# Optimization experiments

Measured on AMD Instinct MI355X. Metric: run time of the kernel, lower is better.

The kernel has to match this reference:

```python
import jax, jax.numpy as jnp
from jax import lax
import numpy as np

B = 2; Hs = 48; Ws = 48
DIM = 768; NH = 6; NP = 4; DH = DIM // NH; HID = int(DIM * 0.25)
LIN = Hs * Ws                    # feat tokens (single deform level)
LQ = 21 * (Hs * Ws) // 4         # query tokens: (2H*2W)+(H*W)+(H/2*W/2)


def _ln(x, g, b, eps=1e-6):
    m = jnp.mean(x, -1, keepdims=True)
    v = jnp.mean((x - m) ** 2, -1, keepdims=True)
    return (x - m) * lax.rsqrt(v + eps) * g + b


def _bilinear_sample(value, loc, Hf, Wf):
    """value: [B,NH,Hf*Wf,DH]; loc: [B,Lq,NH,NP,2] normalized to [0,1].
    Matches F.grid_sample(align_corners=False, padding_mode='zeros')."""
    Bq, nH = value.shape[0], value.shape[1]
    Lq = loc.shape[1]
    x = loc[..., 0] * Wf - 0.5
    y = loc[..., 1] * Hf - 0.5
    x0 = jnp.floor(x); y0 = jnp.floor(y)
    wx1 = x - x0; wy1 = y - y0
    x0i = x0.astype(jnp.int32); y0i = y0.astype(jnp.int32)

    def tr(a):  # [B,Lq,NH,NP] -> [B,NH,Lq*NP]
        return jnp.transpose(a, (0, 2, 1, 3)).reshape(Bq, nH, Lq * NP)

    def gather(yi, xi):
        valid = ((xi >= 0) & (xi < Wf) & (yi >= 0) & (yi < Hf)).astype(value.dtype)
        idx = jnp.clip(yi, 0, Hf - 1) * Wf + jnp.clip(xi, 0, Wf - 1)
        g = jnp.take_along_axis(value, tr(idx)[..., None], axis=2)  # [B,NH,Lq*NP,DH]
        return g * tr(valid)[..., None]

    out = (gather(y0i, x0i) * tr((1 - wy1) * (1 - wx1))[..., None]
         + gather(y0i, x0i + 1) * tr((1 - wy1) * wx1)[..., None]
         + gather(y0i + 1, x0i) * tr(wy1 * (1 - wx1))[..., None]
         + gather(y0i + 1, x0i + 1) * tr(wy1 * wx1)[..., None])
    return out.reshape(Bq, nH, Lq, NP, DH)


def _dwconv(x_tokens, w, b, h, w_):
    Bq, n_tok, C = x_tokens.shape
    img = jnp.transpose(x_tokens, (0, 2, 1)).reshape(Bq, C, h, w_)
    y = lax.conv_general_dilated(img, w, (1, 1), 'SAME',
                                 dimension_numbers=('NCHW', 'OIHW', 'NCHW'),
                                 feature_group_count=C) + b[None, :, None, None]
    return jnp.transpose(y.reshape(Bq, C, h * w_), (0, 2, 1))


def _forward(query, reference_points, feat, qn_g, qn_b, fn_g, fn_b, vW, vb,
             soW, sob, awW, awb, opW, opb, mn_g, mn_b,
             fc1W, fc1b, dwW, dwb, fc2W, fc2b, H, W):
    Bq, Lq, C = query.shape
    q = _ln(query, qn_g, qn_b)
    v = _ln(feat, fn_g, fn_b) @ vW + vb                             # [B,Lin,C]
    value = jnp.transpose(v.reshape(Bq, -1, NH, DH), (0, 2, 1, 3))  # [B,NH,Lin,DH]
    offs = (q @ soW + sob).reshape(Bq, Lq, NH, NP, 2)
    attw = jax.nn.softmax((q @ awW + awb).reshape(Bq, Lq, NH, NP), axis=-1)
    norm = jnp.asarray([W, H], dtype=q.dtype)                       # (x,y) normalizer
    loc = reference_points.reshape(Bq, Lq, 1, 1, 2) + offs / norm   # [B,Lq,NH,NP,2]
    samp = _bilinear_sample(value, loc, H, W)                       # [B,NH,Lq,NP,DH]
    aw = jnp.transpose(attw, (0, 2, 1, 3))[..., None]               # [B,NH,Lq,NP,1]
    out = jnp.sum(samp * aw, axis=3)                                # [B,NH,Lq,DH]
    out = jnp.transpose(out, (0, 2, 1, 3)).reshape(Bq, Lq, C) @ opW + opb
    x = query + out                                                 # residual
    # multi-scale conv MLP
    h = _ln(x, mn_g, mn_b) @ fc1W + fc1b                            # [B,Lq,HID]
    n = Lq // 21
    h = jnp.concatenate([
        _dwconv(h[:, :16 * n], dwW, dwb, 2 * H, 2 * W),
        _dwconv(h[:, 16 * n:20 * n], dwW, dwb, H, W),
        _dwconv(h[:, 20 * n:], dwW, dwb, H // 2, W // 2)], axis=1)
    h = jax.nn.gelu(h, approximate=False)
    h = h @ fc2W + fc2b
    return x + h


def setup_inputs():
    key = jax.random.key(0)
    ks = jax.random.split(key, 16)
    s = 0.02
    return dict(
        query=jax.random.normal(ks[0], (B, LQ, DIM), jnp.float32),
        reference_points=jax.random.uniform(ks[1], (B, LQ, 1, 2), jnp.float32),
        feat=jax.random.normal(ks[2], (B, LIN, DIM), jnp.float32),
        spatial_shapes=jnp.array([[Hs, Ws]], jnp.int32),
        level_start_index=jnp.array([0], jnp.int32),
        H=Hs, W=Ws,
        qn_g=jnp.ones((DIM,)), qn_b=jnp.zeros((DIM,)),
        fn_g=jnp.ones((DIM,)), fn_b=jnp.zeros((DIM,)),
        mn_g=jnp.ones((DIM,)), mn_b=jnp.zeros((DIM,)),
        vW=s * jax.random.normal(ks[3], (DIM, DIM)), vb=jnp.zeros((DIM,)),
        soW=s * jax.random.normal(ks[4], (DIM, NH * NP * 2)),
        sob=0.5 * jax.random.normal(ks[5], (NH * NP * 2,)),
        awW=s * jax.random.normal(ks[6], (DIM, NH * NP)), awb=jnp.zeros((NH * NP,)),
        opW=s * jax.random.normal(ks[7], (DIM, DIM)), opb=jnp.zeros((DIM,)),
        fc1W=s * jax.random.normal(ks[8], (DIM, HID)), fc1b=jnp.zeros((HID,)),
        dwW=s * jax.random.normal(ks[9], (HID, 1, 3, 3)), dwb=jnp.zeros((HID,)),
        fc2W=s * jax.random.normal(ks[10], (HID, DIM)), fc2b=jnp.zeros((DIM,)),
    )


def reference(query, reference_points, feat, spatial_shapes, level_start_index, H, W,
              qn_g, qn_b, fn_g, fn_b, mn_g, mn_b, vW, vb, soW, sob, awW, awb,
              opW, opb, fc1W, fc1b, dwW, dwb, fc2W, fc2b):
    del spatial_shapes, level_start_index  # single level; H,W are static ints
    return _forward(query, reference_points, feat, qn_g, qn_b, fn_g, fn_b, vW, vb,
                    soW, sob, awW, awb, opW, opb, mn_g, mn_b,
                    fc1W, fc1b, dwW, dwb, fc2W, fc2b, H, W)
```

## Files before the change

kernel.cpp:

```cpp
#include <hip/hip_runtime.h>

#define NB    2
#define LQT   12096
#define LINT  2304
#define DIMC  768
#define NHD   6
#define NPT   4
#define DHD   128
#define HIDC  192
#define HH    48
#define WW    48

typedef __attribute__((ext_vector_type(8))) short bf16x8;
typedef __attribute__((ext_vector_type(4))) float f32x4;
typedef __attribute__((ext_vector_type(8))) unsigned short u16x8;

__device__ __forceinline__ unsigned short f2bf(float f) {
  unsigned int u = __builtin_bit_cast(unsigned int, f);
  u += 0x7FFFu + ((u >> 16) & 1u);
  return (unsigned short)(u >> 16);
}

__global__ __launch_bounds__(256) void pack_wt(const float* __restrict__ src,
                                               unsigned short* __restrict__ dst,
                                               int K, int N, int rows) {
  size_t i = (size_t)blockIdx.x * 256 + threadIdx.x;
  if (i >= (size_t)rows * K) return;
  int n = (int)(i / K), k = (int)(i % K);
  float v = (n < N) ? src[(size_t)k * N + n] : 0.f;
  dst[i] = f2bf(v);
}

__global__ __launch_bounds__(256) void pack_soaw(const float* __restrict__ soW,
                                                 const float* __restrict__ awW,
                                                 const float* __restrict__ sob,
                                                 const float* __restrict__ awb,
                                                 unsigned short* __restrict__ dst,
                                                 float* __restrict__ bdst) {
  size_t i = (size_t)blockIdx.x * 256 + threadIdx.x;
  if (i < 128) bdst[i] = (i < 48) ? sob[i] : (i < 72 ? awb[i - 48] : 0.f);
  if (i >= (size_t)128 * DIMC) return;
  int n = (int)(i / DIMC), k = (int)(i % DIMC);
  float v = (n < 48) ? soW[(size_t)k * 48 + n]
                     : (n < 72 ? awW[(size_t)k * 24 + (n - 48)] : 0.f);
  dst[i] = f2bf(v);
}

__global__ __launch_bounds__(256) void ln_to_bf16(const float* __restrict__ in,
                                                  const float* __restrict__ gamma,
                                                  const float* __restrict__ beta,
                                                  unsigned short* __restrict__ out) {
  const int row = blockIdx.x;
  const int t = threadIdx.x;
  const float* x = in + (size_t)row * DIMC;
  float v0 = x[t], v1 = x[t + 256], v2 = x[t + 512];
  float s = v0 + v1 + v2;
  float s2 = v0 * v0 + v1 * v1 + v2 * v2;
#pragma unroll
  for (int o = 32; o > 0; o >>= 1) {
    s += __shfl_down(s, o);
    s2 += __shfl_down(s2, o);
  }
  __shared__ float red[8];
  const int wave = t >> 6, lane = t & 63;
  if (lane == 0) { red[wave] = s; red[wave + 4] = s2; }
  __syncthreads();
  float S = red[0] + red[1] + red[2] + red[3];
  float S2 = red[4] + red[5] + red[6] + red[7];
  float mean = S * (1.0f / DIMC);
  float var = S2 * (1.0f / DIMC) - mean * mean;
  float inv = rsqrtf(var + 1e-6f);
  unsigned short* o0 = out + (size_t)row * DIMC;
  o0[t]       = f2bf((v0 - mean) * inv * gamma[t]       + beta[t]);
  o0[t + 256] = f2bf((v1 - mean) * inv * gamma[t + 256] + beta[t + 256]);
  o0[t + 512] = f2bf((v2 - mean) * inv * gamma[t + 512] + beta[t + 512]);
}

#define LDSS 40
template <bool HAS_ADD>
__global__ __launch_bounds__(256) void gemm_bt(const unsigned short* __restrict__ A,
                                               const unsigned short* __restrict__ Bt,
                                               const float* __restrict__ bias,
                                               const float* __restrict__ add,
                                               float* __restrict__ out,
                                               int M, int N, int K) {
  __shared__ unsigned short As[128 * LDSS];
  __shared__ unsigned short Bs[128 * LDSS];
  const int t = threadIdx.x;
  const int wave = t >> 6, lane = t & 63;
  const int m0 = blockIdx.x * 128;
  const int n0 = blockIdx.y * 128;
  const int wm = (wave >> 1) * 64, wn = (wave & 1) * 64;
  const int lr = lane & 15;
  const int lk = (lane >> 4) * 8;

  const int e0 = t * 8;
  const int r0 = e0 >> 5;
  const int c0 = e0 & 31;

  const size_t arow0 = (size_t)(m0 + r0) * K;
  const size_t arow1 = (size_t)(m0 + r0 + 64) * K;
  const size_t brow0 = (size_t)(n0 + r0) * K;
  const size_t brow1 = (size_t)(n0 + r0 + 64) * K;

  f32x4 acc[4][4] = {};

  for (int k0 = 0; k0 < K; k0 += 32) {
    u16x8 a0 = *(const u16x8*)(A + arow0 + k0 + c0);
    u16x8 a1 = *(const u16x8*)(A + arow1 + k0 + c0);
    u16x8 b0 = *(const u16x8*)(Bt + brow0 + k0 + c0);
    u16x8 b1 = *(const u16x8*)(Bt + brow1 + k0 + c0);
    __syncthreads();
    *(u16x8*)(As + (size_t)r0 * LDSS + c0) = a0;
    *(u16x8*)(As + (size_t)(r0 + 64) * LDSS + c0) = a1;
    *(u16x8*)(Bs + (size_t)r0 * LDSS + c0) = b0;
    *(u16x8*)(Bs + (size_t)(r0 + 64) * LDSS + c0) = b1;
    __syncthreads();
    bf16x8 af[4], bg[4];
#pragma unroll
    for (int i = 0; i < 4; ++i)
      af[i] = *(const bf16x8*)(As + (size_t)(wm + i * 16 + lr) * LDSS + lk);
#pragma unroll
    for (int j = 0; j < 4; ++j)
      bg[j] = *(const bf16x8*)(Bs + (size_t)(wn + j * 16 + lr) * LDSS + lk);
#pragma unroll
    for (int i = 0; i < 4; ++i)
#pragma unroll
      for (int j = 0; j < 4; ++j)
        acc[i][j] = __builtin_amdgcn_mfma_f32_16x16x32_bf16(af[i], bg[j], acc[i][j], 0, 0, 0);
  }

  const int orow = (lane >> 4) * 4;
#pragma unroll
  for (int i = 0; i < 4; ++i) {
#pragma unroll
    for (int j = 0; j < 4; ++j) {
      const int n = n0 + wn + j * 16 + lr;
      if (n < N) {
#pragma unroll
        for (int r = 0; r < 4; ++r) {
          const int m = m0 + wm + i * 16 + orow + r;
          float v = acc[i][j][r] + bias[n];
          if (HAS_ADD) v += add[(size_t)m * N + n];
          out[(size_t)m * N + n] = v;
        }
      }
    }
  }
}

__global__ __launch_bounds__(192) void deform_attn(const float* __restrict__ soaw,
                                                   const float* __restrict__ rp,
                                                   const float* __restrict__ value,
                                                   unsigned short* __restrict__ attn) {
  const int row = blockIdx.x;
  const int b = row / LQT;
  const int t = threadIdx.x;
  const int h = t >> 5;
  const int l = t & 31;
  const float* sa = soaw + (size_t)row * 128;
  const float bx = rp[(size_t)row * 2 + 0] * (float)WW - 0.5f;
  const float by = rp[(size_t)row * 2 + 1] * (float)HH - 0.5f;

  float lg0 = sa[48 + h * 4 + 0], lg1 = sa[48 + h * 4 + 1];
  float lg2 = sa[48 + h * 4 + 2], lg3 = sa[48 + h * 4 + 3];
  float mx = fmaxf(fmaxf(lg0, lg1), fmaxf(lg2, lg3));
  float e0 = expf(lg0 - mx), e1 = expf(lg1 - mx), e2 = expf(lg2 - mx), e3 = expf(lg3 - mx);
  float inv = 1.0f / (e0 + e1 + e2 + e3);
  float awp[4] = {e0 * inv, e1 * inv, e2 * inv, e3 * inv};

  const float* vb = value + (size_t)b * LINT * DIMC + h * DHD + l * 4;
  float ax = 0.f, ay = 0.f, az = 0.f, aw = 0.f;
#pragma unroll
  for (int p = 0; p < 4; ++p) {
    float fx = bx + sa[h * 8 + p * 2 + 0];
    float fy = by + sa[h * 8 + p * 2 + 1];
    float x0f = floorf(fx), y0f = floorf(fy);
    float wx = fx - x0f, wy = fy - y0f;
    int x0 = (int)x0f, y0 = (int)y0f;
#pragma unroll
    for (int dy = 0; dy < 2; ++dy) {
#pragma unroll
      for (int dx = 0; dx < 2; ++dx) {
        int xi = x0 + dx, yi = y0 + dy;
        float w = (dy ? wy : 1.f - wy) * (dx ? wx : 1.f - wx) * awp[p];
        if (xi < 0 || xi >= WW || yi < 0 || yi >= HH) w = 0.f;
        int xc = min(max(xi, 0), WW - 1), yc = min(max(yi, 0), HH - 1);
        const float4 g = *(const float4*)(vb + (size_t)(yc * WW + xc) * DIMC);
        ax += w * g.x; ay += w * g.y; az += w * g.z; aw += w * g.w;
      }
    }
  }
  unsigned short* op = attn + (size_t)row * DIMC + h * DHD + l * 4;
  ushort4 ov;
  ov.x = f2bf(ax); ov.y = f2bf(ay); ov.z = f2bf(az); ov.w = f2bf(aw);
  *(ushort4*)op = ov;
}

__global__ __launch_bounds__(192) void dwconv_gelu(const float* __restrict__ h1,
                                                   const float* __restrict__ dwW,
                                                   const float* __restrict__ dwb,
                                                   unsigned short* __restrict__ out) {
  const int blk = blockIdx.x;
  const int b = blk / LQT;
  const int q = blk % LQT;
  int base, Wi, Hi;
  if (q < 9216)       { base = 0;     Wi = 96; Hi = 96; }
  else if (q < 11520) { base = 9216;  Wi = 48; Hi = 48; }
  else                { base = 11520; Wi = 24; Hi = 24; }
  const int loc = q - base;
  const int y = loc / Wi, x = loc % Wi;
  const int c = threadIdx.x;
  const float* src = h1 + ((size_t)b * LQT + base) * HIDC + c;
  float acc = dwb[c];
#pragma unroll
  for (int dy = -1; dy <= 1; ++dy) {
    int yy = y + dy;
    if (yy < 0 || yy >= Hi) continue;
#pragma unroll
    for (int dx = -1; dx <= 1; ++dx) {
      int xx = x + dx;
      if (xx < 0 || xx >= Wi) continue;
      acc += dwW[c * 9 + (dy + 1) * 3 + (dx + 1)] * src[(size_t)(yy * Wi + xx) * HIDC];
    }
  }
  float g = 0.5f * acc * (1.0f + erff(acc * 0.70710678118654752f));
  out[(size_t)blk * HIDC + c] = f2bf(g);
}

extern "C" void kernel_launch(void* const* d_in, const int* in_sizes, int n_in,
                              void* d_out, int out_size, void* d_ws, size_t ws_size,
                              hipStream_t stream) {
  const float* query = (const float*)d_in[0];
  const float* rp    = (const float*)d_in[1];
  const float* feat  = (const float*)d_in[2];
  const float* qn_g  = (const float*)d_in[7];
  const float* qn_b  = (const float*)d_in[8];
  const float* fn_g  = (const float*)d_in[9];
  const float* fn_b  = (const float*)d_in[10];
  const float* mn_g  = (const float*)d_in[11];
  const float* mn_b  = (const float*)d_in[12];
  const float* vW    = (const float*)d_in[13];
  const float* vb    = (const float*)d_in[14];
  const float* soW   = (const float*)d_in[15];
  const float* sob   = (const float*)d_in[16];
  const float* awW   = (const float*)d_in[17];
  const float* awb   = (const float*)d_in[18];
  const float* opW   = (const float*)d_in[19];
  const float* opb   = (const float*)d_in[20];
  const float* fc1W  = (const float*)d_in[21];
  const float* fc1b  = (const float*)d_in[22];
  const float* dwW   = (const float*)d_in[23];
  const float* dwb   = (const float*)d_in[24];
  const float* fc2W  = (const float*)d_in[25];
  const float* fc2b  = (const float*)d_in[26];
  float* out = (float*)d_out;
  (void)in_sizes; (void)n_in; (void)out_size; (void)ws_size;

  char* ws = (char*)d_ws;
  size_t off = 0;
  auto alloc = [&](size_t bytes) -> void* {
    off = (off + 255) & ~(size_t)255;
    void* p = ws + off;
    off += bytes;
    return p;
  };

  const int MQ = NB * LQT;
  const int MF = NB * LINT;

  unsigned short* vWt    = (unsigned short*)alloc((size_t)768 * 768 * 2);
  unsigned short* opWt   = (unsigned short*)alloc((size_t)768 * 768 * 2);
  unsigned short* soawWt = (unsigned short*)alloc((size_t)128 * 768 * 2);
  unsigned short* fc1Wt  = (unsigned short*)alloc((size_t)256 * 768 * 2);
  unsigned short* fc2Wt  = (unsigned short*)alloc((size_t)768 * 192 * 2);
  float*          soawb  = (float*)alloc(128 * 4);
  unsigned short* f_ln   = (unsigned short*)alloc((size_t)MF * DIMC * 2);
  unsigned short* q_ln   = (unsigned short*)alloc((size_t)MQ * DIMC * 2);
  float*          value  = (float*)alloc((size_t)MF * DIMC * 4);
  float*          soaw   = (float*)alloc((size_t)MQ * 128 * 4);
  unsigned short* attnb  = (unsigned short*)alloc((size_t)MQ * DIMC * 2);
  float*          xbuf   = (float*)alloc((size_t)MQ * DIMC * 4);

  float* h1 = (float*)attnb;
  unsigned short* coutb = (unsigned short*)soaw;
  unsigned short* lnx = q_ln;

  pack_wt<<<dim3((768 * 768 + 255) / 256), dim3(256), 0, stream>>>(vW, vWt, 768, 768, 768);
  pack_wt<<<dim3((768 * 768 + 255) / 256), dim3(256), 0, stream>>>(opW, opWt, 768, 768, 768);
  pack_wt<<<dim3((256 * 768 + 255) / 256), dim3(256), 0, stream>>>(fc1W, fc1Wt, 768, 192, 256);
  pack_wt<<<dim3((768 * 192 + 255) / 256), dim3(256), 0, stream>>>(fc2W, fc2Wt, 192, 768, 768);
  pack_soaw<<<dim3((128 * 768 + 255) / 256), dim3(256), 0, stream>>>(soW, awW, sob, awb, soawWt, soawb);

  ln_to_bf16<<<dim3(MF), dim3(256), 0, stream>>>(feat, fn_g, fn_b, f_ln);
  ln_to_bf16<<<dim3(MQ), dim3(256), 0, stream>>>(query, qn_g, qn_b, q_ln);

  gemm_bt<false><<<dim3(MF / 128, 6), dim3(256), 0, stream>>>(f_ln, vWt, vb, nullptr, value, MF, 768, 768);

  gemm_bt<false><<<dim3(MQ / 128, 1), dim3(256), 0, stream>>>(q_ln, soawWt, soawb, nullptr, soaw, MQ, 128, 768);

  deform_attn<<<dim3(MQ), dim3(192), 0, stream>>>(soaw, rp, value, attnb);

  gemm_bt<true><<<dim3(MQ / 128, 6), dim3(256), 0, stream>>>(attnb, opWt, opb, query, xbuf, MQ, 768, 768);

  ln_to_bf16<<<dim3(MQ), dim3(256), 0, stream>>>(xbuf, mn_g, mn_b, lnx);

  gemm_bt<false><<<dim3(MQ / 128, 2), dim3(256), 0, stream>>>(lnx, fc1Wt, fc1b, nullptr, h1, MQ, 192, 768);

  dwconv_gelu<<<dim3(MQ), dim3(192), 0, stream>>>(h1, dwW, dwb, coutb);

  gemm_bt<true><<<dim3(MQ / 128, 6), dim3(256), 0, stream>>>(coutb, fc2Wt, fc2b, xbuf, out, MQ, 768, 192);
}
```

Before: 367.6 us.

## Use direct global-to-LDS loads with XOR swizzle and K=64 tiles in GEMM

The bf16 GEMM now loads A and B tiles with global_load_lds straight into shared memory instead of staging them through registers. Because that path cannot pad rows, the LDS layout uses an XOR swizzle to avoid bank conflicts, and each iteration covers K=64 instead of 32. This halves the barriers per K and removes register staging, at the cost of double the LDS use, no software double-buffering, and the requirement that K be a multiple of 64.

```diff
diff --git a/kernel.cpp b/kernel.cpp
--- a/kernel.cpp
+++ b/kernel.cpp
@@ -19,6 +19,12 @@
   unsigned int u = __builtin_bit_cast(unsigned int, f);
   u += 0x7FFFu + ((u >> 16) & 1u);
   return (unsigned short)(u >> 16);
+}
+
+__device__ __forceinline__ void gload16(const unsigned short* g, unsigned short* l) {
+  __builtin_amdgcn_global_load_lds(
+      (const __attribute__((address_space(1))) unsigned int*)g,
+      (__attribute__((address_space(3))) unsigned int*)l, 16, 0, 0);
 }
 
 __global__ __launch_bounds__(256) void pack_wt(const float* __restrict__ src,
@@ -76,7 +82,6 @@
   o0[t + 512] = f2bf((v2 - mean) * inv * gamma[t + 512] + beta[t + 512]);
 }
 
-#define LDSS 40
 template <bool HAS_ADD>
 __global__ __launch_bounds__(256) void gemm_bt(const unsigned short* __restrict__ A,
                                                const unsigned short* __restrict__ Bt,
@@ -84,53 +89,55 @@
                                                const float* __restrict__ add,
                                                float* __restrict__ out,
                                                int M, int N, int K) {
-  __shared__ unsigned short As[128 * LDSS];
-  __shared__ unsigned short Bs[128 * LDSS];
+  __shared__ unsigned short As[128 * 64];
+  __shared__ unsigned short Bs[128 * 64];
   const int t = threadIdx.x;
   const int wave = t >> 6, lane = t & 63;
   const int m0 = blockIdx.x * 128;
   const int n0 = blockIdx.y * 128;
   const int wm = (wave >> 1) * 64, wn = (wave & 1) * 64;
   const int lr = lane & 15;
-  const int lk = (lane >> 4) * 8;
-
-  const int e0 = t * 8;
-  const int r0 = e0 >> 5;
-  const int c0 = e0 & 31;
-
-  const size_t arow0 = (size_t)(m0 + r0) * K;
-  const size_t arow1 = (size_t)(m0 + r0 + 64) * K;
-  const size_t brow0 = (size_t)(n0 + r0) * K;
-  const size_t brow1 = (size_t)(n0 + r0 + 64) * K;
+  const int lg = lane >> 4;
+
+  const int srow = wave * 32 + (lane >> 3);
+  const int sslot = lane & 7;
 
   f32x4 acc[4][4] = {};
 
-  for (int k0 = 0; k0 < K; k0 += 32) {
-    u16x8 a0 = *(const u16x8*)(A + arow0 + k0 + c0);
-    u16x8 a1 = *(const u16x8*)(A + arow1 + k0 + c0);
-    u16x8 b0 = *(const u16x8*)(Bt + brow0 + k0 + c0);
-    u16x8 b1 = *(const u16x8*)(Bt + brow1 + k0 + c0);
+  for (int k0 = 0; k0 < K; k0 += 64) {
     __syncthreads();
-    *(u16x8*)(As + (size_t)r0 * LDSS + c0) = a0;
-    *(u16x8*)(As + (size_t)(r0 + 64) * LDSS + c0) = a1;
-    *(u16x8*)(Bs + (size_t)r0 * LDSS + c0) = b0;
-    *(u16x8*)(Bs + (size_t)(r0 + 64) * LDSS + c0) = b1;
+#pragma unroll
+    for (int i = 0; i < 4; ++i) {
+      const int row = srow + i * 8;
+      const int ca = sslot ^ (row & 7);
+      gload16(A  + (size_t)(m0 + row) * K + k0 + ca * 8, As + (wave * 32 + i * 8) * 64);
+      gload16(Bt + (size_t)(n0 + row) * K + k0 + ca * 8, Bs + (wave * 32 + i * 8) * 64);
+    }
     __syncthreads();
-    bf16x8 af[4], bg[4];
-#pragma unroll
-    for (int i = 0; i < 4; ++i)
-      af[i] = *(const bf16x8*)(As + (size_t)(wm + i * 16 + lr) * LDSS + lk);
-#pragma unroll
-    for (int j = 0; j < 4; ++j)
-      bg[j] = *(const bf16x8*)(Bs + (size_t)(wn + j * 16 + lr) * LDSS + lk);
-#pragma unroll
-    for (int i = 0; i < 4; ++i)
-#pragma unroll
-      for (int j = 0; j < 4; ++j)
-        acc[i][j] = __builtin_amdgcn_mfma_f32_16x16x32_bf16(af[i], bg[j], acc[i][j], 0, 0, 0);
-  }
-
-  const int orow = (lane >> 4) * 4;
+
+    bf16x8 af[2][4], bg[2][4];
+#pragma unroll
+    for (int kk = 0; kk < 2; ++kk) {
+#pragma unroll
+      for (int i = 0; i < 4; ++i) {
+        int row = wm + i * 16 + lr;
+        int slot = (kk * 4 + lg) ^ (row & 7);
+        af[kk][i] = *(const bf16x8*)(As + row * 64 + slot * 8);
+        row = wn + i * 16 + lr;
+        slot = (kk * 4 + lg) ^ (row & 7);
+        bg[kk][i] = *(const bf16x8*)(Bs + row * 64 + slot * 8);
+      }
+    }
+#pragma unroll
+    for (int kk = 0; kk < 2; ++kk)
+#pragma unroll
+      for (int i = 0; i < 4; ++i)
+#pragma unroll
+        for (int j = 0; j < 4; ++j)
+          acc[i][j] = __builtin_amdgcn_mfma_f32_16x16x32_bf16(af[kk][i], bg[kk][j], acc[i][j], 0, 0, 0);
+  }
+
+  const int orow = lg * 4;
 #pragma unroll
   for (int i = 0; i < 4; ++i) {
 #pragma unroll
```

After: 346.9 us. -5.6%, faster.
